# Performance work log

Measured on AMD Instinct MI355X. Metric: run time of the kernel, lower is better.

## Reference

```python
import jax, jax.numpy as jnp
import numpy as np
from jax import lax

STRIDES = (8, 8, 16, 32, 32)
GRIDS = (40, 36, 24, 16, 12)
MIN_SCORE = 0.1
KEEP_SCORE = 0.1
MASK_THR = 0.5
UPDATE_THR = 0.05
SIGMA = 2.0
TOPN = 500
MAX_MASKS = 100
UP = 4


def points_nms(h):
    # max_pool2d(k=2, s=1, p=1) then crop last row/col == pad (1,0) window 2
    m = lax.reduce_window(h, -jnp.inf, lax.max, (1, 1, 2, 2), (1, 1, 1, 1),
                          ((0, 0), (0, 0), (1, 0), (1, 0)))
    return h * (m == h).astype(h.dtype)


def resize_mat(insz, outsz):
    # bilinear align_corners=True interpolation matrix [outsz, insz]
    if outsz > 1:
        src = jnp.arange(outsz, dtype=jnp.float32) * ((insz - 1) / (outsz - 1))
    else:
        src = jnp.zeros((outsz,), jnp.float32)
    lo = jnp.clip(jnp.floor(src).astype(jnp.int32), 0, insz - 1)
    hi = jnp.minimum(lo + 1, insz - 1)
    w = src - lo.astype(jnp.float32)
    r = jnp.arange(outsz)
    M = jnp.zeros((outsz, insz), jnp.float32)
    return M.at[r, lo].add(1.0 - w).at[r, hi].add(w)


def bilinear(x, oh, ow):  # x: [k,h,w]
    Mh = resize_mat(x.shape[1], oh)
    Mw = resize_mat(x.shape[2], ow)
    return jnp.einsum('Ww,kHw->kHW', Mw, jnp.einsum('Hh,khw->kHw', Mh, x))


def prep(cate_preds, kernel_preds):
    B = cate_preds[0].shape[0]
    cate = [points_nms(jax.nn.sigmoid(c)) for c in cate_preds]
    cate_flat = jnp.concatenate(
        [jnp.transpose(c, (0, 2, 3, 1)).reshape(B, -1, c.shape[1]) for c in cate], axis=1)
    kern_flat = jnp.concatenate(
        [jnp.transpose(k, (0, 2, 3, 1)).reshape(B, -1, k.shape[1]) for k in kernel_preds], axis=1)
    strides_vec = jnp.concatenate(
        [jnp.full((g * g,), float(s), jnp.float32) for g, s in zip(GRIDS, STRIDES)])
    return cate_flat, kern_flat, strides_vec


def decode_soft(mask_feat, cate_flat, kern_flat, strides_vec):
    # fixed-shape (padded) version of the per-image decode; invalid slots carry score 0
    nc = cate_flat.shape[-1]
    flat = cate_flat.reshape(-1)
    vals, idx = lax.top_k(jnp.where(flat > MIN_SCORE, flat, -1.0), TOPN)
    validk = vals > MIN_SCORE
    cell = idx // nc
    label = idx % nc
    # dynamic 1x1 conv == einsum with gathered kernels
    sig = jax.nn.sigmoid(jnp.einsum('kc,chw->khw', kern_flat[cell], mask_feat))
    binm = (sig > MASK_THR).astype(sig.dtype)
    summ = binm.sum((1, 2))
    keep = validk & (summ > strides_vec[cell])
    seg = (sig * binm).sum((1, 2)) / jnp.maximum(summ, 1e-6)
    scores = jnp.where(keep, vals * seg, 0.0)
    order = jnp.argsort(-scores)
    scores = scores[order]
    sig = sig[order]
    label = label[order]
    keep_o = keep[order]
    summ = jnp.where(keep, summ, 0.0)[order]
    binm = binm[order] * keep_o[:, None, None].astype(binm.dtype)
    # matrix NMS (gaussian)
    flatm = binm.reshape(TOPN, -1)
    inter = flatm @ flatm.T
    iou = inter / jnp.maximum(summ[:, None] + summ[None, :] - inter, 1e-6)
    triu = jnp.triu(jnp.ones((TOPN, TOPN), bool), 1)
    dmat = jnp.where(triu & (label[:, None] == label[None, :]), iou, 0.0)
    comp = dmat.max(0)  # max suppression each item received
    coef = (jnp.exp(-SIGMA * dmat**2) / jnp.exp(-SIGMA * comp[:, None]**2)).min(0)
    s2 = scores * coef
    s2 = jnp.where((s2 >= UPDATE_THR) & (s2 >= KEEP_SCORE) & keep_o, s2, 0.0)
    fv, fi = lax.top_k(s2, MAX_MASKS)
    return fv, jnp.where(fv > 0, label[fi], -1), sig[fi]


def reference(mask_feat_pred, cate_pred_0, cate_pred_1, cate_pred_2, cate_pred_3,
              cate_pred_4, kernel_pred_0, kernel_pred_1, kernel_pred_2, kernel_pred_3,
              kernel_pred_4, scaled_sizes, origin_sizes):
    cate_preds = [cate_pred_0, cate_pred_1, cate_pred_2, cate_pred_3, cate_pred_4]
    kernel_preds = [kernel_pred_0, kernel_pred_1, kernel_pred_2, kernel_pred_3, kernel_pred_4]
    cate_flat, kern_flat, sv = prep(cate_preds, kernel_preds)
    fv, lab, sig = jax.vmap(lambda mf, cf, kf: decode_soft(mf, cf, kf, sv))(
        mask_feat_pred, cate_flat, kern_flat)
    H = mask_feat_pred.shape[2] * UP
    W = mask_feat_pred.shape[3] * UP
    up = jax.vmap(lambda s: bilinear(s, H, W))(sig)  # [B,M,H,W]
    sh, sw = int(scaled_sizes[0, 0]), int(scaled_sizes[0, 1])
    oh, ow = int(origin_sizes[0, 0]), int(origin_sizes[0, 1])
    up = up[:, :, :sh, :sw]
    up = jax.vmap(lambda s: bilinear(s, oh, ow))(up)
    masks = ((up > MASK_THR) & (fv > 0)[:, :, None, None]).astype(jnp.uint8)
    return masks, lab, fv


def setup_inputs() -> dict:
    key = jax.random.key(0)
    ks = jax.random.split(key, 11)
    B, C, NC, HM = 2, 256, 80, 128
    inp = {'mask_feat_pred': jax.random.normal(ks[0], (B, C, HM, HM), jnp.float32)}
    for i, g in enumerate(GRIDS):
        inp[f'cate_pred_{i}'] = jax.random.normal(ks[1 + i], (B, NC, g, g), jnp.float32)
        inp[f'kernel_pred_{i}'] = jax.random.normal(ks[6 + i], (B, C, g, g), jnp.float32) * 0.05
    inp['scaled_sizes'] = jnp.full((B, 2), HM * UP, jnp.int32)
    inp['origin_sizes'] = jnp.full((B, 2), HM * UP, jnp.int32)
    return inp
```

## Files before the change

kernel.cpp:

```cpp
#include <hip/hip_runtime.h>
#include <math.h>
#include <stdint.h>

#define NBATCH 2
#define NC 80
#define CHN 256
#define HMM 128
#define HWN (HMM*HMM)
#define NCELL 3872
#define FLATN (NCELL*NC)
#define TOPN 500
#define SROWS 512
#define MAXM 100
#define OUTH 512
#define OUTW 512
#define NBINS 1024
#define CANDCAP 1024
#define BM 128
#define BN 128
#define BK 16
#define GNB (HWN/BN)

__device__ __forceinline__ float sigmoidf_(float x){ return 1.0f/(1.0f+expf(-x)); }
__device__ __forceinline__ unsigned short f2bf(float x){
  uint32_t u = __float_as_uint(x);
  uint32_t r = u + 0x7FFFu + ((u >> 16) & 1u);
  return (unsigned short)(r >> 16);
}
__device__ __forceinline__ float bf2f(unsigned short h){ return __uint_as_float(((uint32_t)h) << 16); }

__device__ __forceinline__ void cell_decode(int cell, int& lvl, int& g, int& y, int& x){
  int off;
  if (cell < 1600)      { lvl=0; g=40; off=0; }
  else if (cell < 2896) { lvl=1; g=36; off=1600; }
  else if (cell < 3472) { lvl=2; g=24; off=2896; }
  else if (cell < 3728) { lvl=3; g=16; off=3472; }
  else                  { lvl=4; g=12; off=3728; }
  int r = cell - off; y = r / g; x = r - y*g;
}

template<int N, int NT>
__device__ __forceinline__ void bitonic_desc(uint64_t* key){
  int tid = threadIdx.x;
  __syncthreads();
  for (int k = 2; k <= N; k <<= 1)
    for (int j = k >> 1; j > 0; j >>= 1) {
      if (j >= 32) __syncthreads();
      for (int e = tid; e < N; e += NT) {
        int l = e ^ j;
        if (l > e) {
          uint64_t a = key[e], c = key[l];
          bool up = ((e & k) == 0);
          if (up ? (a < c) : (a > c)) { key[e] = c; key[l] = a; }
        }
      }
    }
  __syncthreads();
}

__global__ void k1_scores(const float* __restrict__ c0, const float* __restrict__ c1,
                          const float* __restrict__ c2, const float* __restrict__ c3,
                          const float* __restrict__ c4,
                          float* __restrict__ scores_t, uint32_t* __restrict__ hist){
  int t = blockIdx.x*blockDim.x + threadIdx.x;
  if (t >= NBATCH*FLATN) return;
  int b = t / FLATN;
  int rem = t - b*FLATN;
  int c = rem / NCELL;
  int cell = rem - c*NCELL;
  int lvl,g,y,x; cell_decode(cell,lvl,g,y,x);
  const float* cp = lvl==0?c0:lvl==1?c1:lvl==2?c2:lvl==3?c3:c4;
  const float* base = cp + (size_t)(b*NC + c)*g*g;
  float raw = base[y*g + x];
  float m = raw;
  if (y > 0)          m = fmaxf(m, base[(y-1)*g + x]);
  if (x > 0)          m = fmaxf(m, base[y*g + x-1]);
  if (y > 0 && x > 0) m = fmaxf(m, base[(y-1)*g + x-1]);
  float s = (raw == m) ? sigmoidf_(raw) : 0.0f;
  scores_t[t] = s;
  if (s > 0.1f) {
    int bin = (int)(s * 1024.0f); if (bin > NBINS-1) bin = NBINS-1;
    atomicAdd(&hist[b*NBINS + bin], 1u);
  }
}

__global__ __launch_bounds__(1024) void k2_cutoff(const uint32_t* __restrict__ hist, int* __restrict__ cutoff){
  __shared__ uint32_t h[NBINS];
  int b = blockIdx.x;
  h[threadIdx.x] = hist[b*NBINS + threadIdx.x];
  __syncthreads();
  if (threadIdx.x == 0) {
    int acc = 0; int cut = 0;
    for (int d = NBINS-1; d >= 0; --d) {
      acc += (int)h[d];
      if (acc >= TOPN) { cut = d; break; }
    }
    cutoff[b] = cut;
  }
}

__global__ void k3_gather(const float* __restrict__ scores_t, const int* __restrict__ cutoff,
                          uint32_t* __restrict__ cnt, float* __restrict__ cval, uint32_t* __restrict__ cidx){
  int t = blockIdx.x*blockDim.x + threadIdx.x;
  if (t >= NBATCH*FLATN) return;
  int b = t / FLATN;
  int rem = t - b*FLATN;
  int c = rem / NCELL;
  int cell = rem - c*NCELL;
  float v = scores_t[t];
  if (v > 0.1f) {
    int bin = (int)(v * 1024.0f); if (bin > NBINS-1) bin = NBINS-1;
    if (bin >= cutoff[b]) {
      uint32_t p = atomicAdd(&cnt[b], 1u);
      if (p < CANDCAP) { cval[b*CANDCAP+p] = v; cidx[b*CANDCAP+p] = (uint32_t)(cell*NC + c); }
    }
  }
}

__global__ __launch_bounds__(512) void k4_sort(const uint32_t* __restrict__ cnt,
        const float* __restrict__ cval, const uint32_t* __restrict__ cidx,
        float* __restrict__ vals, int* __restrict__ cellA, int* __restrict__ labelA){
  __shared__ uint64_t key[CANDCAP];
  int b = blockIdx.x; int tid = threadIdx.x;
  int n = (int)cnt[b]; if (n > CANDCAP) n = CANDCAP;
  for (int e = tid; e < CANDCAP; e += 512) {
    uint64_t k = 0;
    if (e < n)
      k = ((uint64_t)__float_as_uint(cval[b*CANDCAP+e]) << 32) |
          (uint64_t)(0xFFFFFFFFu - cidx[b*CANDCAP+e]);
    key[e] = k;
  }
  bitonic_desc<CANDCAP,512>(key);
  for (int r = tid; r < TOPN; r += 512) {
    uint64_t k = key[r];
    if ((k >> 32) == 0) { vals[b*TOPN+r] = -1.0f; cellA[b*TOPN+r] = 0; labelA[b*TOPN+r] = 0; }
    else {
      uint32_t idx = 0xFFFFFFFFu - (uint32_t)(k & 0xFFFFFFFFu);
      vals[b*TOPN+r]   = __uint_as_float((uint32_t)(k >> 32));
      cellA[b*TOPN+r]  = (int)(idx / NC);
      labelA[b*TOPN+r] = (int)(idx % NC);
    }
  }
}

__global__ void k5_kmat(const float* __restrict__ k0p, const float* __restrict__ k1p,
                        const float* __restrict__ k2p, const float* __restrict__ k3p,
                        const float* __restrict__ k4p,
                        const int* __restrict__ cellA, float* __restrict__ Kmat){
  int t = blockIdx.x*blockDim.x + threadIdx.x;
  if (t >= NBATCH*TOPN*CHN) return;
  int b = t / (TOPN*CHN); int rem = t - b*(TOPN*CHN);
  int k = rem / CHN; int c = rem - k*CHN;
  int cell = cellA[b*TOPN + k];
  int lvl,g,y,x; cell_decode(cell,lvl,g,y,x);
  const float* kp = lvl==0?k0p:lvl==1?k1p:lvl==2?k2p:lvl==3?k3p:k4p;
  Kmat[t] = kp[((size_t)(b*CHN + c)*g + y)*g + x];
}

__global__ __launch_bounds__(256) void k6_gemm1(const float* __restrict__ Kmat, const float* __restrict__ mf,
        unsigned short* __restrict__ sigb, uint32_t* __restrict__ bits,
        float* __restrict__ psum, float* __restrict__ pseg){
  __shared__ alignas(16) float As[2][BK][BM+4];
  __shared__ alignas(16) float Bs[2][BK][BN];
  int tid = threadIdx.x;
  int nb = blockIdx.x, mb = blockIdx.y, b = blockIdx.z;
  int row0 = mb*BM, col0 = nb*BN;
  int tx = tid & 15, ty = tid >> 4;

  int ar[2], aq[2], bkk[2], bcc[2];
  #pragma unroll
  for (int i = 0; i < 2; ++i) {
    int e = i*256 + tid;
    ar[i] = e >> 2; aq[i] = e & 3;
    bkk[i] = e >> 5; bcc[i] = e & 31;
  }
  float4 pa[2], pb[2];
  const float4 z4 = make_float4(0.f,0.f,0.f,0.f);
  #pragma unroll
  for (int i = 0; i < 2; ++i) {
    int rr = row0 + ar[i];
    pa[i] = (rr < TOPN) ? *(const float4*)&Kmat[((size_t)b*TOPN + rr)*CHN + aq[i]*4] : z4;
    pb[i] = *(const float4*)&mf[((size_t)b*CHN + bkk[i])*HWN + col0 + bcc[i]*4];
  }
  #pragma unroll
  for (int i = 0; i < 2; ++i) {
    int colA = ar[i] ^ (aq[i] << 2);
    As[0][aq[i]*4+0][colA] = pa[i].x;
    As[0][aq[i]*4+1][colA] = pa[i].y;
    As[0][aq[i]*4+2][colA] = pa[i].z;
    As[0][aq[i]*4+3][colA] = pa[i].w;
    *(float4*)&Bs[0][bkk[i]][bcc[i]*4] = pb[i];
  }
  __syncthreads();

  float acc[8][8];
  #pragma unroll
  for (int i=0;i<8;i++)
    #pragma unroll
    for(int j=0;j<8;j++) acc[i][j]=0.f;

  int cur = 0;
  for (int k0 = 0; k0 < CHN; k0 += BK) {
    bool more = (k0 + BK < CHN);
    if (more) {
      int k0n = k0 + BK;
      #pragma unroll
      for (int i = 0; i < 2; ++i) {
        int rr = row0 + ar[i];
        pa[i] = (rr < TOPN) ? *(const float4*)&Kmat[((size_t)b*TOPN + rr)*CHN + k0n + aq[i]*4] : z4;
        pb[i] = *(const float4*)&mf[((size_t)b*CHN + k0n + bkk[i])*HWN + col0 + bcc[i]*4];
      }
    }
    #pragma unroll 4
    for (int kk = 0; kk < BK; ++kk) {
      int s = (kk >> 2) << 2;
      float4 a0 = *(float4*)&As[cur][kk][(ty*8) ^ s];
      float4 a1 = *(float4*)&As[cur][kk][(ty*8+4) ^ s];
      float4 b0 = *(float4*)&Bs[cur][kk][tx*4];
      float4 b1 = *(float4*)&Bs[cur][kk][64+tx*4];
      float av[8] = {a0.x,a0.y,a0.z,a0.w,a1.x,a1.y,a1.z,a1.w};
      #pragma unroll
      for (int i = 0; i < 8; ++i) {
        acc[i][0] += av[i]*b0.x; acc[i][1] += av[i]*b0.y; acc[i][2] += av[i]*b0.z; acc[i][3] += av[i]*b0.w;
        acc[i][4] += av[i]*b1.x; acc[i][5] += av[i]*b1.y; acc[i][6] += av[i]*b1.z; acc[i][7] += av[i]*b1.w;
      }
    }
    if (more) {
      int nxt = cur ^ 1;
      #pragma unroll
      for (int i = 0; i < 2; ++i) {
        int colA = ar[i] ^ (aq[i] << 2);
        As[nxt][aq[i]*4+0][colA] = pa[i].x;
        As[nxt][aq[i]*4+1][colA] = pa[i].y;
        As[nxt][aq[i]*4+2][colA] = pa[i].z;
        As[nxt][aq[i]*4+3][colA] = pa[i].w;
        *(float4*)&Bs[nxt][bkk[i]][bcc[i]*4] = pb[i];
      }
      __syncthreads();
      cur = nxt;
    }
  }
  #pragma unroll
  for (int i = 0; i < 8; ++i) {
    int r = row0 + ty*8 + i;
    float se = 0.f; int cc = 0;
    #pragma unroll
    for (int q = 0; q < 2; ++q) {
      float4 sv;
      sv.x = sigmoidf_(acc[i][q*4+0]);
      sv.y = sigmoidf_(acc[i][q*4+1]);
      sv.z = sigmoidf_(acc[i][q*4+2]);
      sv.w = sigmoidf_(acc[i][q*4+3]);
      uint32_t m = 0;
      if (sv.x > 0.5f) { m |= 1u; se += sv.x; cc++; }
      if (sv.y > 0.5f) { m |= 2u; se += sv.y; cc++; }
      if (sv.z > 0.5f) { m |= 4u; se += sv.z; cc++; }
      if (sv.w > 0.5f) { m |= 8u; se += sv.w; cc++; }
      uint32_t wrd = m << ((tx & 7)*4);
      wrd |= __shfl_xor(wrd, 1);
      wrd |= __shfl_xor(wrd, 2);
      wrd |= __shfl_xor(wrd, 4);
      if ((tx & 7) == 0 && r < TOPN)
        bits[((size_t)b*TOPN + r)*512 + nb*4 + q*2 + (tx>>3)] = wrd;
      ushort4 sb;
      sb.x = f2bf(sv.x); sb.y = f2bf(sv.y); sb.z = f2bf(sv.z); sb.w = f2bf(sv.w);
      *(ushort4*)&sigb[((size_t)b*SROWS + r)*HWN + col0 + q*64 + tx*4] = sb;
    }
    #pragma unroll
    for (int d = 1; d < 16; d <<= 1) {
      se += __shfl_xor(se, d);
      cc += __shfl_xor(cc, d);
    }
    if (tx == 0 && r < TOPN) {
      psum[(size_t)nb*(NBATCH*TOPN) + b*TOPN + r] = (float)cc;
      pseg[(size_t)nb*(NBATCH*TOPN) + b*TOPN + r] = se;
    }
  }
}

__global__ __launch_bounds__(512) void k78_stats_order(const float* __restrict__ psum, const float* __restrict__ pseg,
        const float* __restrict__ vals, const int* __restrict__ cellA,
        float* __restrict__ summ, float* __restrict__ scores, int* __restrict__ keepA,
        int* __restrict__ order, float* __restrict__ comp){
  __shared__ uint64_t key[512];
  int b = blockIdx.x, tid = threadIdx.x;
  uint64_t k = 0;
  if (tid < TOPN) {
    int t = b*TOPN + tid;
    comp[t] = 0.f;
    float sc = 0.f, sg = 0.f;
    for (int i = 0; i < GNB; ++i) {
      sc += psum[(size_t)i*(NBATCH*TOPN) + t];
      sg += pseg[(size_t)i*(NBATCH*TOPN) + t];
    }
    float v = vals[t];
    int cell = cellA[t];
    int lvl,g,y,x; cell_decode(cell,lvl,g,y,x);
    float stride = (lvl<=1)?8.f:(lvl==2)?16.f:32.f;
    bool keep = (v > 0.1f) && (sc > stride);
    float seg = sg / fmaxf(sc, 1e-6f);
    summ[t] = sc;
    float s = keep ? v*seg : 0.f;
    scores[t] = s;
    keepA[t] = keep ? 1 : 0;
    k = ((uint64_t)__float_as_uint(s) << 32) | (uint64_t)(0xFFFFFFFFu - (uint32_t)tid);
  }
  key[tid] = k;
  bitonic_desc<512,512>(key);
  if (tid < TOPN) order[b*TOPN+tid] = (int)(0xFFFFFFFFu - (uint32_t)(key[tid] & 0xFFFFFFFFu));
}

__global__ __launch_bounds__(256) void k9_dmat(const uint32_t* __restrict__ bitsG,
        const int* __restrict__ order, const int* __restrict__ labelA, const int* __restrict__ keepA,
        const float* __restrict__ summ, float* __restrict__ dmatT, float* __restrict__ comp){
  __shared__ uint32_t rowb[512];
  int i = blockIdx.x, b = blockIdx.y, tid = threadIdx.x;
  int oi = order[b*TOPN + i];
  if (!keepA[b*TOPN + oi]) return;
  float si = summ[b*TOPN + oi];
  int li = labelA[b*TOPN + oi];
  for (int w = tid; w < 512; w += 256) rowb[w] = bitsG[((size_t)b*TOPN + oi)*512 + w];
  __syncthreads();
  for (int j = i + 1 + tid; j < TOPN; j += 256) {
    int oj = order[b*TOPN + j];
    if (!keepA[b*TOPN + oj] || labelA[b*TOPN + oj] != li) continue;
    const uint4* rj = (const uint4*)&bitsG[((size_t)b*TOPN + oj)*512];
    const uint4* ri = (const uint4*)rowb;
    int cc = 0;
    for (int w = 0; w < 128; ++w) {
      uint4 x = rj[w], y = ri[w];
      cc += __popc(x.x & y.x) + __popc(x.y & y.y) + __popc(x.z & y.z) + __popc(x.w & y.w);
    }
    float sj = summ[b*TOPN + oj];
    float inter = (float)cc;
    float v = inter / fmaxf(si + sj - inter, 1e-6f);
    dmatT[((size_t)b*TOPN + j)*TOPN + i] = v;
    if (v > 0.f) atomicMax((int*)&comp[b*TOPN + j], __float_as_int(v));
  }
}

__global__ __launch_bounds__(256) void k10_coef(const float* __restrict__ dmatT, const float* __restrict__ comp,
        const float* __restrict__ scores, const int* __restrict__ order, const int* __restrict__ keepA,
        float* __restrict__ s2){
  __shared__ float red[4];
  int j = blockIdx.x, b = blockIdx.y, tid = threadIdx.x;
  float mn = 1e30f;
  for (int i = tid; i < TOPN; i += 256) {
    float d = dmatT[((size_t)b*TOPN+j)*TOPN + i];
    float c = comp[b*TOPN+i];
    float r = expf(-2.0f*d*d) / expf(-2.0f*c*c);
    mn = fminf(mn, r);
  }
  #pragma unroll
  for (int d = 1; d < 64; d <<= 1) mn = fminf(mn, __shfl_xor(mn, d));
  if ((tid & 63) == 0) red[tid >> 6] = mn;
  __syncthreads();
  if (tid == 0) {
    mn = fminf(fminf(red[0], red[1]), fminf(red[2], red[3]));
    int oj = order[b*TOPN+j];
    float s = scores[b*TOPN+oj] * mn;
    bool ok = (s >= 0.05f) && (s >= 0.1f) && (keepA[b*TOPN+oj] != 0);
    s2[b*TOPN+j] = ok ? s : 0.f;
  }
}

__global__ __launch_bounds__(512) void k11_top100(const float* __restrict__ s2, const int* __restrict__ order,
        const int* __restrict__ labelA, float* __restrict__ outF, int* __restrict__ selrow){
  __shared__ uint64_t key[512];
  int b = blockIdx.x, tid = threadIdx.x;
  uint64_t k = 0;
  if (tid < TOPN)
    k = ((uint64_t)__float_as_uint(s2[b*TOPN+tid]) << 32) | (uint64_t)(0xFFFFFFFFu - (uint32_t)tid);
  key[tid] = k;
  bitonic_desc<512,512>(key);
  if (tid < MAXM) {
    uint64_t kk = key[tid];
    float v = __uint_as_float((uint32_t)(kk >> 32));
    int j = (int)(0xFFFFFFFFu - (uint32_t)(kk & 0xFFFFFFFFu));
    if (j < 0 || j >= TOPN) { j = 0; v = 0.f; }
    int orow = order[b*TOPN + j];
    float lab = (v > 0.f) ? (float)labelA[b*TOPN + orow] : -1.0f;
    size_t maskCount = (size_t)NBATCH*MAXM*OUTH*OUTW;
    outF[maskCount + (size_t)b*MAXM + tid] = lab;
    outF[maskCount + (size_t)NBATCH*MAXM + (size_t)b*MAXM + tid] = v;
    selrow[b*MAXM + tid] = orow;
  }
}

__global__ void k13_upsample(const unsigned short* __restrict__ sigb, const int* __restrict__ selrow,
                             float* __restrict__ outF){
  int t = blockIdx.x*blockDim.x + threadIdx.x;
  const int XG = OUTW/4;
  int total = NBATCH*MAXM*OUTH*XG;
  if (t >= total) return;
  int xg = t % XG;
  int tmp = t / XG;
  int Y = tmp % OUTH;
  int tmp2 = tmp / OUTH;
  int r = tmp2 % MAXM;
  int b = tmp2 / MAXM;
  size_t maskCount = (size_t)NBATCH*MAXM*OUTH*OUTW;
  float fv = outF[maskCount + (size_t)NBATCH*MAXM + (size_t)b*MAXM + r];
  float4 o = make_float4(0.f,0.f,0.f,0.f);
  if (fv > 0.f) {
    const unsigned short* sm = sigb + ((size_t)b*SROWS + selrow[b*MAXM + r])*HWN;
    const float SC = (float)(127.0/511.0);
    float fy = (float)Y * SC;
    int ly = (int)floorf(fy); if (ly < 0) ly = 0; if (ly > HMM-1) ly = HMM-1;
    int hy = ly+1 < HMM ? ly+1 : HMM-1;
    float wy = fy - (float)ly;
    float res[4];
    #pragma unroll
    for (int u = 0; u < 4; ++u) {
      int X = xg*4 + u;
      float fx = (float)X * SC;
      int lx = (int)floorf(fx); if (lx < 0) lx = 0; if (lx > HMM-1) lx = HMM-1;
      int hx = lx+1 < HMM ? lx+1 : HMM-1;
      float wx = fx - (float)lx;
      float a = (1.f-wy)*bf2f(sm[ly*HMM+lx]) + wy*bf2f(sm[hy*HMM+lx]);
      float c = (1.f-wy)*bf2f(sm[ly*HMM+hx]) + wy*bf2f(sm[hy*HMM+hx]);
      float v = (1.f-wx)*a + wx*c;
      res[u] = (v > 0.5f) ? 1.f : 0.f;
    }
    o = make_float4(res[0],res[1],res[2],res[3]);
  }
  *(float4*)&outF[(((size_t)b*MAXM + r)*OUTH + Y)*OUTW + xg*4] = o;
}

extern "C" void kernel_launch(void* const* d_in, const int* in_sizes, int n_in,
                              void* d_out, int out_size, void* d_ws, size_t ws_size,
                              hipStream_t stream) {
  const float* mf = (const float*)d_in[0];
  const float *cate[5], *kern[5];
  bool interleaved = (n_in > 2) && (in_sizes[2] == NBATCH*CHN*40*40);
  if (interleaved) {
    for (int i = 0; i < 5; ++i) { cate[i] = (const float*)d_in[1 + 2*i]; kern[i] = (const float*)d_in[2 + 2*i]; }
  } else {
    for (int i = 0; i < 5; ++i) { cate[i] = (const float*)d_in[1 + i]; kern[i] = (const float*)d_in[6 + i]; }
  }
  float* outF = (float*)d_out;

  uint8_t* p = (uint8_t*)d_ws;
  auto alloc = [&](size_t bytes) -> void* {
    void* r = (void*)p;
    p += (bytes + 255) & ~(size_t)255;
    return r;
  };
  uint8_t*  zbase       = p;
  uint32_t* hist        = (uint32_t*)alloc((size_t)(NBATCH*NBINS + NBATCH)*4);
  uint32_t* cnt         = hist + NBATCH*NBINS;
  float*    dmatT       = (float*)   alloc((size_t)NBATCH*TOPN*TOPN*4);
  size_t    zbytes      = (size_t)(p - zbase);

  float*    scores_t    = (float*)   alloc((size_t)NBATCH*FLATN*4);
  int*      cutoff      = (int*)     alloc((size_t)NBATCH*4);
  float*    cval        = (float*)   alloc((size_t)NBATCH*CANDCAP*4);
  uint32_t* cidx        = (uint32_t*)alloc((size_t)NBATCH*CANDCAP*4);
  float*    vals        = (float*)   alloc((size_t)NBATCH*TOPN*4);
  int*      cellA       = (int*)     alloc((size_t)NBATCH*TOPN*4);
  int*      labelA      = (int*)     alloc((size_t)NBATCH*TOPN*4);
  float*    Kmat        = (float*)   alloc((size_t)NBATCH*TOPN*CHN*4);
  uint32_t* bits        = (uint32_t*)alloc((size_t)NBATCH*TOPN*512*4);
  float*    psum        = (float*)   alloc((size_t)GNB*NBATCH*TOPN*4);
  float*    pseg        = (float*)   alloc((size_t)GNB*NBATCH*TOPN*4);
  float*    summ        = (float*)   alloc((size_t)NBATCH*TOPN*4);
  float*    scores      = (float*)   alloc((size_t)NBATCH*TOPN*4);
  int*      keepA       = (int*)     alloc((size_t)NBATCH*TOPN*4);
  int*      order       = (int*)     alloc((size_t)NBATCH*TOPN*4);
  float*    comp        = (float*)   alloc((size_t)NBATCH*TOPN*4);
  float*    s2          = (float*)   alloc((size_t)NBATCH*TOPN*4);
  int*      selrow      = (int*)     alloc((size_t)NBATCH*MAXM*4);
  unsigned short* sigb  = (unsigned short*)alloc((size_t)NBATCH*SROWS*HWN*2);
  (void)ws_size; (void)out_size;

  hipMemsetAsync(zbase, 0, zbytes, stream);
  hipLaunchKernelGGL(k1_scores, dim3((NBATCH*FLATN + 255)/256), dim3(256), 0, stream,
                     cate[0], cate[1], cate[2], cate[3], cate[4], scores_t, hist);
  hipLaunchKernelGGL(k2_cutoff, dim3(NBATCH), dim3(1024), 0, stream, hist, cutoff);
  hipLaunchKernelGGL(k3_gather, dim3((NBATCH*FLATN + 255)/256), dim3(256), 0, stream,
                     scores_t, cutoff, cnt, cval, cidx);
  hipLaunchKernelGGL(k4_sort, dim3(NBATCH), dim3(512), 0, stream, cnt, cval, cidx, vals, cellA, labelA);
  hipLaunchKernelGGL(k5_kmat, dim3((NBATCH*TOPN*CHN + 255)/256), dim3(256), 0, stream,
                     kern[0], kern[1], kern[2], kern[3], kern[4], cellA, Kmat);
  hipLaunchKernelGGL(k6_gemm1, dim3(GNB, (TOPN+BM-1)/BM, NBATCH), dim3(256), 0, stream,
                     Kmat, mf, sigb, bits, psum, pseg);
  hipLaunchKernelGGL(k78_stats_order, dim3(NBATCH), dim3(512), 0, stream,
                     psum, pseg, vals, cellA, summ, scores, keepA, order, comp);
  hipLaunchKernelGGL(k9_dmat, dim3(TOPN, NBATCH), dim3(256), 0, stream,
                     bits, order, labelA, keepA, summ, dmatT, comp);
  hipLaunchKernelGGL(k10_coef, dim3(TOPN, NBATCH), dim3(256), 0, stream,
                     dmatT, comp, scores, order, keepA, s2);
  hipLaunchKernelGGL(k11_top100, dim3(NBATCH), dim3(512), 0, stream, s2, order, labelA, outF, selrow);
  hipLaunchKernelGGL(k13_upsample, dim3((NBATCH*MAXM*OUTH*(OUTW/4) + 255)/256), dim3(256), 0, stream,
                     sigb, selrow, outF);
}
```

Measured before the change: 375.1 us.

## Fuse small serial kernels via last-block-done pattern and drop dmat memset

Merges the histogram cutoff into the score kernel, the top-k sort into the gather kernel, and the top-100 selection into the coefficient kernel. Each merged kernel uses an atomic counter so the last finishing block does the serial tail work. This removes three launches and their gaps. The decay matrix is now written in full by the dmat kernel, including zeros, and read column-wise, so it no longer needs to be part of the zeroed memset region. The cost is a serial tail inside one block plus extra fence and atomic traffic.

```diff
diff --git a/kernel.cpp b/kernel.cpp
--- a/kernel.cpp
+++ b/kernel.cpp
@@ -61,85 +61,102 @@
 __global__ void k1_scores(const float* __restrict__ c0, const float* __restrict__ c1,
                           const float* __restrict__ c2, const float* __restrict__ c3,
                           const float* __restrict__ c4,
-                          float* __restrict__ scores_t, uint32_t* __restrict__ hist){
-  int t = blockIdx.x*blockDim.x + threadIdx.x;
-  if (t >= NBATCH*FLATN) return;
-  int b = t / FLATN;
-  int rem = t - b*FLATN;
-  int c = rem / NCELL;
-  int cell = rem - c*NCELL;
-  int lvl,g,y,x; cell_decode(cell,lvl,g,y,x);
-  const float* cp = lvl==0?c0:lvl==1?c1:lvl==2?c2:lvl==3?c3:c4;
-  const float* base = cp + (size_t)(b*NC + c)*g*g;
-  float raw = base[y*g + x];
-  float m = raw;
-  if (y > 0)          m = fmaxf(m, base[(y-1)*g + x]);
-  if (x > 0)          m = fmaxf(m, base[y*g + x-1]);
-  if (y > 0 && x > 0) m = fmaxf(m, base[(y-1)*g + x-1]);
-  float s = (raw == m) ? sigmoidf_(raw) : 0.0f;
-  scores_t[t] = s;
-  if (s > 0.1f) {
-    int bin = (int)(s * 1024.0f); if (bin > NBINS-1) bin = NBINS-1;
-    atomicAdd(&hist[b*NBINS + bin], 1u);
-  }
-}
-
-__global__ __launch_bounds__(1024) void k2_cutoff(const uint32_t* __restrict__ hist, int* __restrict__ cutoff){
+                          float* __restrict__ scores_t, uint32_t* __restrict__ hist,
+                          uint32_t* __restrict__ ctr, int* __restrict__ cutoff){
   __shared__ uint32_t h[NBINS];
-  int b = blockIdx.x;
-  h[threadIdx.x] = hist[b*NBINS + threadIdx.x];
-  __syncthreads();
-  if (threadIdx.x == 0) {
-    int acc = 0; int cut = 0;
-    for (int d = NBINS-1; d >= 0; --d) {
-      acc += (int)h[d];
-      if (acc >= TOPN) { cut = d; break; }
-    }
-    cutoff[b] = cut;
-  }
-}
-
-__global__ void k3_gather(const float* __restrict__ scores_t, const int* __restrict__ cutoff,
-                          uint32_t* __restrict__ cnt, float* __restrict__ cval, uint32_t* __restrict__ cidx){
-  int t = blockIdx.x*blockDim.x + threadIdx.x;
-  if (t >= NBATCH*FLATN) return;
-  int b = t / FLATN;
-  int rem = t - b*FLATN;
-  int c = rem / NCELL;
-  int cell = rem - c*NCELL;
-  float v = scores_t[t];
-  if (v > 0.1f) {
-    int bin = (int)(v * 1024.0f); if (bin > NBINS-1) bin = NBINS-1;
-    if (bin >= cutoff[b]) {
-      uint32_t p = atomicAdd(&cnt[b], 1u);
-      if (p < CANDCAP) { cval[b*CANDCAP+p] = v; cidx[b*CANDCAP+p] = (uint32_t)(cell*NC + c); }
-    }
-  }
-}
-
-__global__ __launch_bounds__(512) void k4_sort(const uint32_t* __restrict__ cnt,
-        const float* __restrict__ cval, const uint32_t* __restrict__ cidx,
+  __shared__ int lastF;
+  int tid = threadIdx.x;
+  int t = blockIdx.x*blockDim.x + tid;
+  if (t < NBATCH*FLATN) {
+    int b = t / FLATN;
+    int rem = t - b*FLATN;
+    int c = rem / NCELL;
+    int cell = rem - c*NCELL;
+    int lvl,g,y,x; cell_decode(cell,lvl,g,y,x);
+    const float* cp = lvl==0?c0:lvl==1?c1:lvl==2?c2:lvl==3?c3:c4;
+    const float* base = cp + (size_t)(b*NC + c)*g*g;
+    float raw = base[y*g + x];
+    float m = raw;
+    if (y > 0)          m = fmaxf(m, base[(y-1)*g + x]);
+    if (x > 0)          m = fmaxf(m, base[y*g + x-1]);
+    if (y > 0 && x > 0) m = fmaxf(m, base[(y-1)*g + x-1]);
+    float s = (raw == m) ? sigmoidf_(raw) : 0.0f;
+    scores_t[t] = s;
+    if (s > 0.1f) {
+      int bin = (int)(s * 1024.0f); if (bin > NBINS-1) bin = NBINS-1;
+      atomicAdd(&hist[b*NBINS + bin], 1u);
+    }
+  }
+  __threadfence();
+  __syncthreads();
+  if (tid == 0) lastF = (atomicAdd(ctr, 1u) == gridDim.x - 1) ? 1 : 0;
+  __syncthreads();
+  if (!lastF) return;
+  for (int b2 = 0; b2 < NBATCH; ++b2) {
+    for (int i = tid; i < NBINS; i += 256) h[i] = atomicAdd(&hist[b2*NBINS + i], 0u);
+    __syncthreads();
+    if (tid == 0) {
+      int acc = 0; int cut = 0;
+      for (int d = NBINS-1; d >= 0; --d) {
+        acc += (int)h[d];
+        if (acc >= TOPN) { cut = d; break; }
+      }
+      cutoff[b2] = cut;
+    }
+    __syncthreads();
+  }
+}
+
+__global__ __launch_bounds__(512) void k3_gather(const float* __restrict__ scores_t, const int* __restrict__ cutoff,
+        uint32_t* __restrict__ cnt, float* __restrict__ cval, uint32_t* __restrict__ cidx,
+        uint32_t* __restrict__ ctr,
         float* __restrict__ vals, int* __restrict__ cellA, int* __restrict__ labelA){
   __shared__ uint64_t key[CANDCAP];
-  int b = blockIdx.x; int tid = threadIdx.x;
-  int n = (int)cnt[b]; if (n > CANDCAP) n = CANDCAP;
-  for (int e = tid; e < CANDCAP; e += 512) {
-    uint64_t k = 0;
-    if (e < n)
-      k = ((uint64_t)__float_as_uint(cval[b*CANDCAP+e]) << 32) |
-          (uint64_t)(0xFFFFFFFFu - cidx[b*CANDCAP+e]);
-    key[e] = k;
-  }
-  bitonic_desc<CANDCAP,512>(key);
-  for (int r = tid; r < TOPN; r += 512) {
-    uint64_t k = key[r];
-    if ((k >> 32) == 0) { vals[b*TOPN+r] = -1.0f; cellA[b*TOPN+r] = 0; labelA[b*TOPN+r] = 0; }
-    else {
-      uint32_t idx = 0xFFFFFFFFu - (uint32_t)(k & 0xFFFFFFFFu);
-      vals[b*TOPN+r]   = __uint_as_float((uint32_t)(k >> 32));
-      cellA[b*TOPN+r]  = (int)(idx / NC);
-      labelA[b*TOPN+r] = (int)(idx % NC);
-    }
+  __shared__ int lastF;
+  int tid = threadIdx.x;
+  int t = blockIdx.x*blockDim.x + tid;
+  if (t < NBATCH*FLATN) {
+    int b = t / FLATN;
+    int rem = t - b*FLATN;
+    int c = rem / NCELL;
+    int cell = rem - c*NCELL;
+    float v = scores_t[t];
+    if (v > 0.1f) {
+      int bin = (int)(v * 1024.0f); if (bin > NBINS-1) bin = NBINS-1;
+      if (bin >= cutoff[b]) {
+        uint32_t p = atomicAdd(&cnt[b], 1u);
+        if (p < CANDCAP) { cval[b*CANDCAP+p] = v; cidx[b*CANDCAP+p] = (uint32_t)(cell*NC + c); }
+      }
+    }
+  }
+  __threadfence();
+  __syncthreads();
+  if (tid == 0) lastF = (atomicAdd(ctr, 1u) == gridDim.x - 1) ? 1 : 0;
+  __syncthreads();
+  if (!lastF) return;
+  for (int b2 = 0; b2 < NBATCH; ++b2) {
+    int n = (int)atomicAdd(&cnt[b2], 0u); if (n > CANDCAP) n = CANDCAP;
+    for (int e = tid; e < CANDCAP; e += 512) {
+      uint64_t k = 0;
+      if (e < n) {
+        float v = atomicAdd(&cval[b2*CANDCAP+e], 0.0f);
+        uint32_t ix = atomicAdd(&cidx[b2*CANDCAP+e], 0u);
+        k = ((uint64_t)__float_as_uint(v) << 32) | (uint64_t)(0xFFFFFFFFu - ix);
+      }
+      key[e] = k;
+    }
+    bitonic_desc<CANDCAP,512>(key);
+    for (int r = tid; r < TOPN; r += 512) {
+      uint64_t k = key[r];
+      if ((k >> 32) == 0) { vals[b2*TOPN+r] = -1.0f; cellA[b2*TOPN+r] = 0; labelA[b2*TOPN+r] = 0; }
+      else {
+        uint32_t idx = 0xFFFFFFFFu - (uint32_t)(k & 0xFFFFFFFFu);
+        vals[b2*TOPN+r]   = __uint_as_float((uint32_t)(k >> 32));
+        cellA[b2*TOPN+r]  = (int)(idx / NC);
+        labelA[b2*TOPN+r] = (int)(idx % NC);
+      }
+    }
+    __syncthreads();
   }
 }
 
@@ -312,78 +329,92 @@
 
 __global__ __launch_bounds__(256) void k9_dmat(const uint32_t* __restrict__ bitsG,
         const int* __restrict__ order, const int* __restrict__ labelA, const int* __restrict__ keepA,
-        const float* __restrict__ summ, float* __restrict__ dmatT, float* __restrict__ comp){
+        const float* __restrict__ summ, float* __restrict__ dmat, float* __restrict__ comp){
   __shared__ uint32_t rowb[512];
   int i = blockIdx.x, b = blockIdx.y, tid = threadIdx.x;
   int oi = order[b*TOPN + i];
-  if (!keepA[b*TOPN + oi]) return;
+  int keep_i = keepA[b*TOPN + oi];
   float si = summ[b*TOPN + oi];
   int li = labelA[b*TOPN + oi];
-  for (int w = tid; w < 512; w += 256) rowb[w] = bitsG[((size_t)b*TOPN + oi)*512 + w];
-  __syncthreads();
-  for (int j = i + 1 + tid; j < TOPN; j += 256) {
-    int oj = order[b*TOPN + j];
-    if (!keepA[b*TOPN + oj] || labelA[b*TOPN + oj] != li) continue;
-    const uint4* rj = (const uint4*)&bitsG[((size_t)b*TOPN + oj)*512];
-    const uint4* ri = (const uint4*)rowb;
-    int cc = 0;
-    for (int w = 0; w < 128; ++w) {
-      uint4 x = rj[w], y = ri[w];
-      cc += __popc(x.x & y.x) + __popc(x.y & y.y) + __popc(x.z & y.z) + __popc(x.w & y.w);
-    }
-    float sj = summ[b*TOPN + oj];
-    float inter = (float)cc;
-    float v = inter / fmaxf(si + sj - inter, 1e-6f);
-    dmatT[((size_t)b*TOPN + j)*TOPN + i] = v;
+  if (keep_i)
+    for (int w = tid; w < 512; w += 256) rowb[w] = bitsG[((size_t)b*TOPN + oi)*512 + w];
+  __syncthreads();
+  float* drow = dmat + ((size_t)b*TOPN + i)*TOPN;
+  for (int j = tid; j < TOPN; j += 256) {
+    float v = 0.f;
+    if (keep_i && j > i) {
+      int oj = order[b*TOPN + j];
+      if (keepA[b*TOPN + oj] && labelA[b*TOPN + oj] == li) {
+        const uint4* rj = (const uint4*)&bitsG[((size_t)b*TOPN + oj)*512];
+        const uint4* ri = (const uint4*)rowb;
+        int cc = 0;
+        for (int w = 0; w < 128; ++w) {
+          uint4 x = rj[w], y = ri[w];
+          cc += __popc(x.x & y.x) + __popc(x.y & y.y) + __popc(x.z & y.z) + __popc(x.w & y.w);
+        }
+        float sj = summ[b*TOPN + oj];
+        float inter = (float)cc;
+        v = inter / fmaxf(si + sj - inter, 1e-6f);
+      }
+    }
+    drow[j] = v;
     if (v > 0.f) atomicMax((int*)&comp[b*TOPN + j], __float_as_int(v));
   }
 }
 
-__global__ __launch_bounds__(256) void k10_coef(const float* __restrict__ dmatT, const float* __restrict__ comp,
+__global__ __launch_bounds__(512) void k10_coef(const float* __restrict__ dmat, const float* __restrict__ comp,
         const float* __restrict__ scores, const int* __restrict__ order, const int* __restrict__ keepA,
-        float* __restrict__ s2){
-  __shared__ float red[4];
+        const int* __restrict__ labelA,
+        float* __restrict__ s2, uint32_t* __restrict__ ctr,
+        float* __restrict__ outF, int* __restrict__ selrow){
+  __shared__ float red[8];
+  __shared__ uint64_t key[512];
+  __shared__ int lastF;
   int j = blockIdx.x, b = blockIdx.y, tid = threadIdx.x;
   float mn = 1e30f;
-  for (int i = tid; i < TOPN; i += 256) {
-    float d = dmatT[((size_t)b*TOPN+j)*TOPN + i];
-    float c = comp[b*TOPN+i];
-    float r = expf(-2.0f*d*d) / expf(-2.0f*c*c);
-    mn = fminf(mn, r);
+  if (tid < TOPN) {
+    float d = dmat[((size_t)b*TOPN + tid)*TOPN + j];
+    float c = comp[b*TOPN + tid];
+    mn = expf(-2.0f*d*d) / expf(-2.0f*c*c);
   }
   #pragma unroll
   for (int d = 1; d < 64; d <<= 1) mn = fminf(mn, __shfl_xor(mn, d));
   if ((tid & 63) == 0) red[tid >> 6] = mn;
   __syncthreads();
   if (tid == 0) {
-    mn = fminf(fminf(red[0], red[1]), fminf(red[2], red[3]));
+    mn = red[0];
+    #pragma unroll
+    for (int w = 1; w < 8; ++w) mn = fminf(mn, red[w]);
     int oj = order[b*TOPN+j];
     float s = scores[b*TOPN+oj] * mn;
     bool ok = (s >= 0.05f) && (s >= 0.1f) && (keepA[b*TOPN+oj] != 0);
     s2[b*TOPN+j] = ok ? s : 0.f;
-  }
-}
-
-__global__ __launch_bounds__(512) void k11_top100(const float* __restrict__ s2, const int* __restrict__ order,
-        const int* __restrict__ labelA, float* __restrict__ outF, int* __restrict__ selrow){
-  __shared__ uint64_t key[512];
-  int b = blockIdx.x, tid = threadIdx.x;
-  uint64_t k = 0;
-  if (tid < TOPN)
-    k = ((uint64_t)__float_as_uint(s2[b*TOPN+tid]) << 32) | (uint64_t)(0xFFFFFFFFu - (uint32_t)tid);
-  key[tid] = k;
-  bitonic_desc<512,512>(key);
-  if (tid < MAXM) {
-    uint64_t kk = key[tid];
-    float v = __uint_as_float((uint32_t)(kk >> 32));
-    int j = (int)(0xFFFFFFFFu - (uint32_t)(kk & 0xFFFFFFFFu));
-    if (j < 0 || j >= TOPN) { j = 0; v = 0.f; }
-    int orow = order[b*TOPN + j];
-    float lab = (v > 0.f) ? (float)labelA[b*TOPN + orow] : -1.0f;
-    size_t maskCount = (size_t)NBATCH*MAXM*OUTH*OUTW;
-    outF[maskCount + (size_t)b*MAXM + tid] = lab;
-    outF[maskCount + (size_t)NBATCH*MAXM + (size_t)b*MAXM + tid] = v;
-    selrow[b*MAXM + tid] = orow;
+    __threadfence();
+    lastF = (atomicAdd(ctr, 1u) == (uint32_t)(TOPN*NBATCH - 1)) ? 1 : 0;
+  }
+  __syncthreads();
+  if (!lastF) return;
+  for (int b2 = 0; b2 < NBATCH; ++b2) {
+    uint64_t k = 0;
+    if (tid < TOPN) {
+      float v = atomicAdd((float*)&s2[b2*TOPN + tid], 0.0f);
+      k = ((uint64_t)__float_as_uint(v) << 32) | (uint64_t)(0xFFFFFFFFu - (uint32_t)tid);
+    }
+    key[tid] = k;
+    bitonic_desc<512,512>(key);
+    if (tid < MAXM) {
+      uint64_t kk = key[tid];
+      float v = __uint_as_float((uint32_t)(kk >> 32));
+      int jj = (int)(0xFFFFFFFFu - (uint32_t)(kk & 0xFFFFFFFFu));
+      if (jj < 0 || jj >= TOPN) { jj = 0; v = 0.f; }
+      int orow = order[b2*TOPN + jj];
+      float lab = (v > 0.f) ? (float)labelA[b2*TOPN + orow] : -1.0f;
+      size_t maskCount = (size_t)NBATCH*MAXM*OUTH*OUTW;
+      outF[maskCount + (size_t)b2*MAXM + tid] = lab;
+      outF[maskCount + (size_t)NBATCH*MAXM + (size_t)b2*MAXM + tid] = v;
+      selrow[b2*MAXM + tid] = orow;
+    }
+    __syncthreads();
   }
 }
 
@@ -447,9 +478,11 @@
     return r;
   };
   uint8_t*  zbase       = p;
-  uint32_t* hist        = (uint32_t*)alloc((size_t)(NBATCH*NBINS + NBATCH)*4);
+  uint32_t* hist        = (uint32_t*)alloc((size_t)(NBATCH*NBINS + NBATCH + 4)*4);
   uint32_t* cnt         = hist + NBATCH*NBINS;
-  float*    dmatT       = (float*)   alloc((size_t)NBATCH*TOPN*TOPN*4);
+  uint32_t* ctr1        = cnt + NBATCH;
+  uint32_t* ctr3        = ctr1 + 1;
+  uint32_t* ctr10       = ctr3 + 1;
   size_t    zbytes      = (size_t)(p - zbase);
 
   float*    scores_t    = (float*)   alloc((size_t)NBATCH*FLATN*4);
@@ -467,6 +500,7 @@
   float*    scores      = (float*)   alloc((size_t)NBATCH*TOPN*4);
   int*      keepA       = (int*)     alloc((size_t)NBATCH*TOPN*4);
   int*      order       = (int*)     alloc((size_t)NBATCH*TOPN*4);
+  float*    dmat        = (float*)   alloc((size_t)NBATCH*TOPN*TOPN*4);
   float*    comp        = (float*)   alloc((size_t)NBATCH*TOPN*4);
   float*    s2          = (float*)   alloc((size_t)NBATCH*TOPN*4);
   int*      selrow      = (int*)     alloc((size_t)NBATCH*MAXM*4);
@@ -475,11 +509,9 @@
 
   hipMemsetAsync(zbase, 0, zbytes, stream);
   hipLaunchKernelGGL(k1_scores, dim3((NBATCH*FLATN + 255)/256), dim3(256), 0, stream,
-                     cate[0], cate[1], cate[2], cate[3], cate[4], scores_t, hist);
-  hipLaunchKernelGGL(k2_cutoff, dim3(NBATCH), dim3(1024), 0, stream, hist, cutoff);
-  hipLaunchKernelGGL(k3_gather, dim3((NBATCH*FLATN + 255)/256), dim3(256), 0, stream,
-                     scores_t, cutoff, cnt, cval, cidx);
-  hipLaunchKernelGGL(k4_sort, dim3(NBATCH), dim3(512), 0, stream, cnt, cval, cidx, vals, cellA, labelA);
+                     cate[0], cate[1], cate[2], cate[3], cate[4], scores_t, hist, ctr1, cutoff);
+  hipLaunchKernelGGL(k3_gather, dim3((NBATCH*FLATN + 511)/512), dim3(512), 0, stream,
+                     scores_t, cutoff, cnt, cval, cidx, ctr3, vals, cellA, labelA);
   hipLaunchKernelGGL(k5_kmat, dim3((NBATCH*TOPN*CHN + 255)/256), dim3(256), 0, stream,
                      kern[0], kern[1], kern[2], kern[3], kern[4], cellA, Kmat);
   hipLaunchKernelGGL(k6_gemm1, dim3(GNB, (TOPN+BM-1)/BM, NBATCH), dim3(256), 0, stream,
@@ -487,10 +519,9 @@
   hipLaunchKernelGGL(k78_stats_order, dim3(NBATCH), dim3(512), 0, stream,
                      psum, pseg, vals, cellA, summ, scores, keepA, order, comp);
   hipLaunchKernelGGL(k9_dmat, dim3(TOPN, NBATCH), dim3(256), 0, stream,
-                     bits, order, labelA, keepA, summ, dmatT, comp);
-  hipLaunchKernelGGL(k10_coef, dim3(TOPN, NBATCH), dim3(256), 0, stream,
-                     dmatT, comp, scores, order, keepA, s2);
-  hipLaunchKernelGGL(k11_top100, dim3(NBATCH), dim3(512), 0, stream, s2, order, labelA, outF, selrow);
+                     bits, order, labelA, keepA, summ, dmat, comp);
+  hipLaunchKernelGGL(k10_coef, dim3(TOPN, NBATCH), dim3(512), 0, stream,
+                     dmat, comp, scores, order, keepA, labelA, s2, ctr10, outF, selrow);
   hipLaunchKernelGGL(k13_upsample, dim3((NBATCH*MAXM*OUTH*(OUTW/4) + 255)/256), dim3(256), 0, stream,
                      sigb, selrow, outF);
 }
```

Result: slower. 651.1 us (+73.6%).

## Privatize score histogram in LDS and drop dmat memset via coalesced row writes

Applied to the files above, without the earlier changes.

The score kernel now builds a per-block shared-memory histogram and flushes nonzero bins to global memory with one atomic each, which cuts global atomic contention. The IoU matrix is now written row-major and fully, with explicit zeros, by k9, so it leaves the memset region and the 2MB zeroing goes away. k10 reads it column-wise with 512 threads, one element per thread. The column reads in k10 are strided and uncoalesced, which could offset the savings from dropping the memset.

```diff
diff --git a/kernel.cpp b/kernel.cpp
--- a/kernel.cpp
+++ b/kernel.cpp
@@ -62,25 +62,35 @@
                           const float* __restrict__ c2, const float* __restrict__ c3,
                           const float* __restrict__ c4,
                           float* __restrict__ scores_t, uint32_t* __restrict__ hist){
-  int t = blockIdx.x*blockDim.x + threadIdx.x;
-  if (t >= NBATCH*FLATN) return;
-  int b = t / FLATN;
-  int rem = t - b*FLATN;
-  int c = rem / NCELL;
-  int cell = rem - c*NCELL;
-  int lvl,g,y,x; cell_decode(cell,lvl,g,y,x);
-  const float* cp = lvl==0?c0:lvl==1?c1:lvl==2?c2:lvl==3?c3:c4;
-  const float* base = cp + (size_t)(b*NC + c)*g*g;
-  float raw = base[y*g + x];
-  float m = raw;
-  if (y > 0)          m = fmaxf(m, base[(y-1)*g + x]);
-  if (x > 0)          m = fmaxf(m, base[y*g + x-1]);
-  if (y > 0 && x > 0) m = fmaxf(m, base[(y-1)*g + x-1]);
-  float s = (raw == m) ? sigmoidf_(raw) : 0.0f;
-  scores_t[t] = s;
-  if (s > 0.1f) {
-    int bin = (int)(s * 1024.0f); if (bin > NBINS-1) bin = NBINS-1;
-    atomicAdd(&hist[b*NBINS + bin], 1u);
+  __shared__ uint32_t h[NBATCH*NBINS];
+  int tid = threadIdx.x;
+  for (int i = tid; i < NBATCH*NBINS; i += 256) h[i] = 0;
+  __syncthreads();
+  int t = blockIdx.x*blockDim.x + tid;
+  if (t < NBATCH*FLATN) {
+    int b = t / FLATN;
+    int rem = t - b*FLATN;
+    int c = rem / NCELL;
+    int cell = rem - c*NCELL;
+    int lvl,g,y,x; cell_decode(cell,lvl,g,y,x);
+    const float* cp = lvl==0?c0:lvl==1?c1:lvl==2?c2:lvl==3?c3:c4;
+    const float* base = cp + (size_t)(b*NC + c)*g*g;
+    float raw = base[y*g + x];
+    float m = raw;
+    if (y > 0)          m = fmaxf(m, base[(y-1)*g + x]);
+    if (x > 0)          m = fmaxf(m, base[y*g + x-1]);
+    if (y > 0 && x > 0) m = fmaxf(m, base[(y-1)*g + x-1]);
+    float s = (raw == m) ? sigmoidf_(raw) : 0.0f;
+    scores_t[t] = s;
+    if (s > 0.1f) {
+      int bin = (int)(s * 1024.0f); if (bin > NBINS-1) bin = NBINS-1;
+      atomicAdd(&h[b*NBINS + bin], 1u);
+    }
+  }
+  __syncthreads();
+  for (int i = tid; i < NBATCH*NBINS; i += 256) {
+    uint32_t v = h[i];
+    if (v) atomicAdd(&hist[i], v);
   }
 }
 
@@ -312,51 +322,58 @@
 
 __global__ __launch_bounds__(256) void k9_dmat(const uint32_t* __restrict__ bitsG,
         const int* __restrict__ order, const int* __restrict__ labelA, const int* __restrict__ keepA,
-        const float* __restrict__ summ, float* __restrict__ dmatT, float* __restrict__ comp){
+        const float* __restrict__ summ, float* __restrict__ dmat, float* __restrict__ comp){
   __shared__ uint32_t rowb[512];
   int i = blockIdx.x, b = blockIdx.y, tid = threadIdx.x;
   int oi = order[b*TOPN + i];
-  if (!keepA[b*TOPN + oi]) return;
+  int keep_i = keepA[b*TOPN + oi];
   float si = summ[b*TOPN + oi];
   int li = labelA[b*TOPN + oi];
-  for (int w = tid; w < 512; w += 256) rowb[w] = bitsG[((size_t)b*TOPN + oi)*512 + w];
-  __syncthreads();
-  for (int j = i + 1 + tid; j < TOPN; j += 256) {
-    int oj = order[b*TOPN + j];
-    if (!keepA[b*TOPN + oj] || labelA[b*TOPN + oj] != li) continue;
-    const uint4* rj = (const uint4*)&bitsG[((size_t)b*TOPN + oj)*512];
-    const uint4* ri = (const uint4*)rowb;
-    int cc = 0;
-    for (int w = 0; w < 128; ++w) {
-      uint4 x = rj[w], y = ri[w];
-      cc += __popc(x.x & y.x) + __popc(x.y & y.y) + __popc(x.z & y.z) + __popc(x.w & y.w);
-    }
-    float sj = summ[b*TOPN + oj];
-    float inter = (float)cc;
-    float v = inter / fmaxf(si + sj - inter, 1e-6f);
-    dmatT[((size_t)b*TOPN + j)*TOPN + i] = v;
+  if (keep_i)
+    for (int w = tid; w < 512; w += 256) rowb[w] = bitsG[((size_t)b*TOPN + oi)*512 + w];
+  __syncthreads();
+  float* drow = dmat + ((size_t)b*TOPN + i)*TOPN;
+  for (int j = tid; j < TOPN; j += 256) {
+    float v = 0.f;
+    if (keep_i && j > i) {
+      int oj = order[b*TOPN + j];
+      if (keepA[b*TOPN + oj] && labelA[b*TOPN + oj] == li) {
+        const uint4* rj = (const uint4*)&bitsG[((size_t)b*TOPN + oj)*512];
+        const uint4* ri = (const uint4*)rowb;
+        int cc = 0;
+        for (int w = 0; w < 128; ++w) {
+          uint4 x = rj[w], y = ri[w];
+          cc += __popc(x.x & y.x) + __popc(x.y & y.y) + __popc(x.z & y.z) + __popc(x.w & y.w);
+        }
+        float sj = summ[b*TOPN + oj];
+        float inter = (float)cc;
+        v = inter / fmaxf(si + sj - inter, 1e-6f);
+      }
+    }
+    drow[j] = v;
     if (v > 0.f) atomicMax((int*)&comp[b*TOPN + j], __float_as_int(v));
   }
 }
 
-__global__ __launch_bounds__(256) void k10_coef(const float* __restrict__ dmatT, const float* __restrict__ comp,
+__global__ __launch_bounds__(512) void k10_coef(const float* __restrict__ dmat, const float* __restrict__ comp,
         const float* __restrict__ scores, const int* __restrict__ order, const int* __restrict__ keepA,
         float* __restrict__ s2){
-  __shared__ float red[4];
+  __shared__ float red[8];
   int j = blockIdx.x, b = blockIdx.y, tid = threadIdx.x;
   float mn = 1e30f;
-  for (int i = tid; i < TOPN; i += 256) {
-    float d = dmatT[((size_t)b*TOPN+j)*TOPN + i];
-    float c = comp[b*TOPN+i];
-    float r = expf(-2.0f*d*d) / expf(-2.0f*c*c);
-    mn = fminf(mn, r);
+  if (tid < TOPN) {
+    float d = dmat[((size_t)b*TOPN + tid)*TOPN + j];
+    float c = comp[b*TOPN + tid];
+    mn = expf(-2.0f*d*d) / expf(-2.0f*c*c);
   }
   #pragma unroll
   for (int d = 1; d < 64; d <<= 1) mn = fminf(mn, __shfl_xor(mn, d));
   if ((tid & 63) == 0) red[tid >> 6] = mn;
   __syncthreads();
   if (tid == 0) {
-    mn = fminf(fminf(red[0], red[1]), fminf(red[2], red[3]));
+    mn = red[0];
+    #pragma unroll
+    for (int w = 1; w < 8; ++w) mn = fminf(mn, red[w]);
     int oj = order[b*TOPN+j];
     float s = scores[b*TOPN+oj] * mn;
     bool ok = (s >= 0.05f) && (s >= 0.1f) && (keepA[b*TOPN+oj] != 0);
@@ -449,7 +466,6 @@
   uint8_t*  zbase       = p;
   uint32_t* hist        = (uint32_t*)alloc((size_t)(NBATCH*NBINS + NBATCH)*4);
   uint32_t* cnt         = hist + NBATCH*NBINS;
-  float*    dmatT       = (float*)   alloc((size_t)NBATCH*TOPN*TOPN*4);
   size_t    zbytes      = (size_t)(p - zbase);
 
   float*    scores_t    = (float*)   alloc((size_t)NBATCH*FLATN*4);
@@ -467,6 +483,7 @@
   float*    scores      = (float*)   alloc((size_t)NBATCH*TOPN*4);
   int*      keepA       = (int*)     alloc((size_t)NBATCH*TOPN*4);
   int*      order       = (int*)     alloc((size_t)NBATCH*TOPN*4);
+  float*    dmat        = (float*)   alloc((size_t)NBATCH*TOPN*TOPN*4);
   float*    comp        = (float*)   alloc((size_t)NBATCH*TOPN*4);
   float*    s2          = (float*)   alloc((size_t)NBATCH*TOPN*4);
   int*      selrow      = (int*)     alloc((size_t)NBATCH*MAXM*4);
@@ -487,9 +504,9 @@
   hipLaunchKernelGGL(k78_stats_order, dim3(NBATCH), dim3(512), 0, stream,
                      psum, pseg, vals, cellA, summ, scores, keepA, order, comp);
   hipLaunchKernelGGL(k9_dmat, dim3(TOPN, NBATCH), dim3(256), 0, stream,
-                     bits, order, labelA, keepA, summ, dmatT, comp);
-  hipLaunchKernelGGL(k10_coef, dim3(TOPN, NBATCH), dim3(256), 0, stream,
-                     dmatT, comp, scores, order, keepA, s2);
+                     bits, order, labelA, keepA, summ, dmat, comp);
+  hipLaunchKernelGGL(k10_coef, dim3(TOPN, NBATCH), dim3(512), 0, stream,
+                     dmat, comp, scores, order, keepA, s2);
   hipLaunchKernelGGL(k11_top100, dim3(NBATCH), dim3(512), 0, stream, s2, order, labelA, outF, selrow);
   hipLaunchKernelGGL(k13_upsample, dim3((NBATCH*MAXM*OUTH*(OUTW/4) + 255)/256), dim3(256), 0, stream,
                      sigb, selrow, outF);
```

Result: faster. 340.7 us, median of 2 (-9.2%).
